# Optimization experiments

Measured on AMD Instinct MI355X. Metric: run time of the kernel, lower is better.

## Reference

```python
import jax, jax.numpy as jnp
import numpy as np

VOCAB_SIZE = 32000


def setup_inputs() -> dict:
    key = jax.random.key(0)
    k1, k2, k3, k4 = jax.random.split(key, 4)
    B, S, T, H = 4, 512, 256, 1024
    return {
        "inputs": jax.random.randint(k1, (B, S), 0, VOCAB_SIZE, dtype=jnp.int32),
        "encoder_outputs": jax.random.normal(k2, (B, S, H), dtype=jnp.float32),
        "decoder_outputs": jax.random.normal(k3, (B, T, H), dtype=jnp.float32),
        "input_bias": jnp.zeros((B, S), dtype=jnp.float32),
        "W_proj": jax.random.normal(k4, (H, H), dtype=jnp.float32) * (1.0 / np.sqrt(H)),
        "b_proj": jnp.zeros((H,), dtype=jnp.float32),
    }


def reference(inputs, encoder_outputs, decoder_outputs, input_bias, W_proj, b_proj):
    # copy_projection: Dense(hidden) with tanh activation on encoder outputs
    enc = jnp.tanh(jnp.einsum("bsh,hk->bsk", encoder_outputs, W_proj) + b_proj)
    # decoder-encoder scores: [B, T, S]
    scores = jnp.einsum("bth,bsh->bts", decoder_outputs, enc)
    scores = scores + input_bias[:, None, :]  # bias broadcast over target dim
    probs = jax.nn.softmax(scores, axis=-1)  # [B, T, S]

    # map_updates_to_vocab: scatter-add probs into vocab slots by token id
    def scatter_one(p, ids):  # p: [T, S], ids: [S]
        return jnp.zeros((p.shape[0], VOCAB_SIZE), p.dtype).at[:, ids].add(p)

    copy_probs = jax.vmap(scatter_one)(probs, inputs)  # [B, T, V]
    return copy_probs
```

## Files before the change

kernel.cpp:

```cpp
#include <hip/hip_runtime.h>
#include <hip/hip_bf16.h>
#include <math.h>

typedef __bf16 bf16x8 __attribute__((ext_vector_type(8)));
typedef float  f32x4  __attribute__((ext_vector_type(4)));

__device__ __forceinline__ unsigned short f2bf(float x) {
    unsigned u = __float_as_uint(x);
    u += 0x7fffu + ((u >> 16) & 1u);
    return (unsigned short)(u >> 16);
}
__device__ __forceinline__ float bf2f(unsigned short h) {
    return __uint_as_float(((unsigned)h) << 16);
}

__device__ __forceinline__ void gl2lds16(const void* g, void* l) {
    __builtin_amdgcn_global_load_lds(
        (const __attribute__((address_space(1))) unsigned int*)(uintptr_t)g,
        (__attribute__((address_space(3))) unsigned int*)(unsigned int)(uintptr_t)l,
        16, 0, 0);
}

__global__ __launch_bounds__(256) void prep(const float* __restrict__ encf,
                                            unsigned short* __restrict__ eh,
                                            unsigned short* __restrict__ el,
                                            const float* __restrict__ decf,
                                            unsigned short* __restrict__ dh,
                                            unsigned short* __restrict__ dl,
                                            const float* __restrict__ W,
                                            unsigned short* __restrict__ Wth,
                                            unsigned short* __restrict__ Wtl) {
    const int bid = blockIdx.x;
    if (bid < 3072) {
        const float* src; unsigned short *ph, *pl; int i;
        if (bid < 2048) { src = encf; ph = eh; pl = el; i = bid * 256 + threadIdx.x; }
        else            { src = decf; ph = dh; pl = dl; i = (bid - 2048) * 256 + threadIdx.x; }
        const float4 v = ((const float4*)src)[i];
        ushort4 h, l;
        h.x = f2bf(v.x); l.x = f2bf(v.x - bf2f(h.x));
        h.y = f2bf(v.y); l.y = f2bf(v.y - bf2f(h.y));
        h.z = f2bf(v.z); l.z = f2bf(v.z - bf2f(h.z));
        h.w = f2bf(v.w); l.w = f2bf(v.w - bf2f(h.w));
        ((ushort4*)ph)[i] = h;
        ((ushort4*)pl)[i] = l;
        return;
    }
    __shared__ float tile[64][65];
    const int tb = bid - 3072;
    const int k0 = (tb >> 4) * 64, n0 = (tb & 15) * 64;
    const int c = threadIdx.x & 63, r0 = threadIdx.x >> 6;
    #pragma unroll
    for (int p = 0; p < 16; ++p) {
        int r = r0 + p * 4;
        tile[r][c] = W[(size_t)(k0 + r) * 1024 + n0 + c];
    }
    __syncthreads();
    #pragma unroll
    for (int p = 0; p < 16; ++p) {
        int rn = r0 + p * 4;
        float v = tile[c][rn];
        unsigned short h = f2bf(v);
        size_t idx = (size_t)(n0 + rn) * 1024 + k0 + c;
        Wth[idx] = h;
        Wtl[idx] = f2bf(v - bf2f(h));
    }
}

template <int EPI>
__global__ __launch_bounds__(256) void gemm128(
    const unsigned short* __restrict__ Ah, const unsigned short* __restrict__ Al,
    const unsigned short* __restrict__ Bh, const unsigned short* __restrict__ Bl,
    const float* __restrict__ bias,
    float* __restrict__ Cf, unsigned short* __restrict__ Ch, unsigned short* __restrict__ Cl,
    int N, int K, int kIter, int ksplit,
    long long aBatch, long long bBatch, long long cBatch, long long cPart) {

    const int z = blockIdx.z;
    const int batch = z / ksplit;
    const int ks = z - batch * ksplit;
    Ah += (size_t)batch * aBatch;  Al += (size_t)batch * aBatch;
    Bh += (size_t)batch * bBatch;  Bl += (size_t)batch * bBatch;
    const int kOff = ks * kIter * 32;

    __shared__ __align__(16) unsigned short sAh[128 * 32];
    __shared__ __align__(16) unsigned short sAl[128 * 32];
    __shared__ __align__(16) unsigned short sBh[128 * 32];
    __shared__ __align__(16) unsigned short sBl[128 * 32];

    const int t = threadIdx.x;
    const int lane = t & 63;
    const int w = t >> 6;
    const int wm = w >> 1, wn = w & 1;
    const int ln15 = lane & 15, q4 = lane >> 4;

    const int row0 = blockIdx.y * 128;
    const int col0 = blockIdx.x * 128;

    const int c0 = t,        r0s = c0 >> 2, g0 = ((c0 & 3) ^ (r0s & 3) ^ ((r0s >> 2) & 3)) * 8;
    const int c1 = t + 256,  r1s = c1 >> 2, g1 = ((c1 & 3) ^ (r1s & 3) ^ ((r1s >> 2) & 3)) * 8;
    const size_t a0 = (size_t)(row0 + r0s) * K + kOff + g0;
    const size_t a1 = (size_t)(row0 + r1s) * K + kOff + g1;
    const size_t b0 = (size_t)(col0 + r0s) * K + kOff + g0;
    const size_t b1 = (size_t)(col0 + r1s) * K + kOff + g1;

    const int pq = (q4 ^ (ln15 & 3) ^ ((ln15 >> 2) & 3)) * 8;

    f32x4 acc[4][4] = {};

    for (int kk = 0; kk < kIter; ++kk) {
        const int k0 = kk * 32;
        gl2lds16(Ah + a0 + k0, &sAh[c0 * 8]);
        gl2lds16(Ah + a1 + k0, &sAh[c1 * 8]);
        gl2lds16(Al + a0 + k0, &sAl[c0 * 8]);
        gl2lds16(Al + a1 + k0, &sAl[c1 * 8]);
        gl2lds16(Bh + b0 + k0, &sBh[c0 * 8]);
        gl2lds16(Bh + b1 + k0, &sBh[c1 * 8]);
        gl2lds16(Bl + b0 + k0, &sBl[c0 * 8]);
        gl2lds16(Bl + b1 + k0, &sBl[c1 * 8]);
        __syncthreads();

        bf16x8 ah[4], al[4], bh[4], bl[4];
        #pragma unroll
        for (int i = 0; i < 4; ++i) {
            int rr = wm * 64 + i * 16 + ln15;
            ah[i] = *(const bf16x8*)&sAh[rr * 32 + pq];
            al[i] = *(const bf16x8*)&sAl[rr * 32 + pq];
        }
        #pragma unroll
        for (int j = 0; j < 4; ++j) {
            int rr = wn * 64 + j * 16 + ln15;
            bh[j] = *(const bf16x8*)&sBh[rr * 32 + pq];
            bl[j] = *(const bf16x8*)&sBl[rr * 32 + pq];
        }
        #pragma unroll
        for (int i = 0; i < 4; ++i)
            #pragma unroll
            for (int j = 0; j < 4; ++j) {
                acc[i][j] = __builtin_amdgcn_mfma_f32_16x16x32_bf16(ah[i], bh[j], acc[i][j], 0, 0, 0);
                acc[i][j] = __builtin_amdgcn_mfma_f32_16x16x32_bf16(ah[i], bl[j], acc[i][j], 0, 0, 0);
                acc[i][j] = __builtin_amdgcn_mfma_f32_16x16x32_bf16(al[i], bh[j], acc[i][j], 0, 0, 0);
            }
        __syncthreads();
    }

    float* outp = (EPI == 0) ? (Cf + (size_t)batch * cBatch + (size_t)ks * cPart) : nullptr;
    #pragma unroll
    for (int i = 0; i < 4; ++i)
        #pragma unroll
        for (int j = 0; j < 4; ++j) {
            int colg = col0 + wn * 64 + j * 16 + ln15;
            float bv = (EPI == 1) ? bias[colg] : 0.0f;
            #pragma unroll
            for (int r = 0; r < 4; ++r) {
                int rowg = row0 + wm * 64 + i * 16 + q4 * 4 + r;
                if (EPI == 0) {
                    outp[(size_t)rowg * N + colg] = acc[i][j][r];
                } else {
                    float tv = tanhf(acc[i][j][r] + bv);
                    unsigned short h = f2bf(tv);
                    size_t idx = (size_t)rowg * N + colg;
                    Ch[idx] = h;
                    Cl[idx] = f2bf(tv - bf2f(h));
                }
            }
        }
}

__inline__ __device__ float waveReduceMax(float v) {
    #pragma unroll
    for (int off = 32; off > 0; off >>= 1) v = fmaxf(v, __shfl_down(v, off));
    return v;
}
__inline__ __device__ float waveReduceSum(float v) {
    #pragma unroll
    for (int off = 32; off > 0; off >>= 1) v += __shfl_down(v, off);
    return v;
}

__global__ __launch_bounds__(256) void softmax_scatter(const float* __restrict__ scores,
                                                       const int* __restrict__ tokens,
                                                       const float* __restrict__ ibias,
                                                       float* __restrict__ out) {
    const int row = blockIdx.x;
    const int b = row >> 8;
    const size_t plane = (size_t)4 * 256 * 512;
    const float* s0 = scores + (size_t)row * 512;
    const float* bi = ibias + (size_t)b * 512;
    const int* tok = tokens + (size_t)b * 512;
    float* o = out + (size_t)row * 32000;

    __shared__ float red[4];
    const int tid = threadIdx.x;
    const int wid = tid >> 6, lane = tid & 63;

    float v0 = bi[tid], v1 = bi[tid + 256];
    #pragma unroll
    for (int p = 0; p < 4; ++p) {
        v0 += s0[p * plane + tid];
        v1 += s0[p * plane + tid + 256];
    }

    float m = fmaxf(v0, v1);
    m = waveReduceMax(m);
    if (lane == 0) red[wid] = m;
    __syncthreads();
    if (tid == 0) red[0] = fmaxf(fmaxf(red[0], red[1]), fmaxf(red[2], red[3]));
    __syncthreads();
    const float rowmax = red[0];
    __syncthreads();

    float e0 = __expf(v0 - rowmax);
    float e1 = __expf(v1 - rowmax);
    float s = e0 + e1;
    s = waveReduceSum(s);
    if (lane == 0) red[wid] = s;
    __syncthreads();
    if (tid == 0) red[0] = red[0] + red[1] + red[2] + red[3];
    __syncthreads();
    const float inv = 1.0f / red[0];

    float4 z = make_float4(0.f, 0.f, 0.f, 0.f);
    float4* o4 = (float4*)o;
    for (int i = tid; i < 8000; i += 256) o4[i] = z;

    __threadfence_block();
    __syncthreads();

    atomicAdd(&o[tok[tid]],       e0 * inv);
    atomicAdd(&o[tok[tid + 256]], e1 * inv);
}

extern "C" void kernel_launch(void* const* d_in, const int* in_sizes, int n_in,
                              void* d_out, int out_size, void* d_ws, size_t ws_size,
                              hipStream_t stream) {
    const int*   inputs  = (const int*)d_in[0];
    const float* enc_in  = (const float*)d_in[1];
    const float* dec_in  = (const float*)d_in[2];
    const float* ibias   = (const float*)d_in[3];
    const float* W       = (const float*)d_in[4];
    const float* bproj   = (const float*)d_in[5];
    float* out = (float*)d_out;

    float* scores = (float*)d_ws;

    size_t outBytes = (size_t)out_size * sizeof(float);
    char* tail = (char*)d_out + outBytes - (size_t)24 * 1024 * 1024;
    unsigned short* Aeh = (unsigned short*)tail;
    unsigned short* Ael = Aeh + (size_t)2048 * 1024;
    unsigned short* Dh  = Ael + (size_t)2048 * 1024;
    unsigned short* Dl  = Dh  + (size_t)1024 * 1024;
    unsigned short* Wth = Dl  + (size_t)1024 * 1024;
    unsigned short* Wtl = Wth + (size_t)1024 * 1024;
    unsigned short* ench = Wtl + (size_t)1024 * 1024;
    unsigned short* encl = ench + (size_t)2048 * 1024;

    prep<<<dim3(3328), 256, 0, stream>>>(enc_in, Aeh, Ael, dec_in, Dh, Dl, W, Wth, Wtl);

    gemm128<1><<<dim3(8, 16, 1), 256, 0, stream>>>(
        Aeh, Ael, Wth, Wtl, bproj, nullptr, ench, encl,
        1024, 1024, 32, 1, 0LL, 0LL, 0LL, 0LL);

    gemm128<0><<<dim3(4, 2, 16), 256, 0, stream>>>(
        Dh, Dl, ench, encl, nullptr, scores, nullptr, nullptr,
        512, 1024, 8, 4,
        (long long)256 * 1024, (long long)512 * 1024,
        (long long)256 * 512, (long long)4 * 256 * 512);

    softmax_scatter<<<dim3(4 * 256), 256, 0, stream>>>(scores, inputs, ibias, out);
}
```

Before: 242.0 us.

## Replace LDS-staged GEMM with direct global-to-register MFMA fragment loads

Both split-bf16 GEMMs now skip shared memory. Each wave loads its MFMA fragments directly from global memory, on a new tiling of 256x32 per block and 64x32 per wave, with two k-steps unrolled and no barriers. This removes the LDS staging and the syncthreads cost and gives more blocks. In exchange, data reuse across waves drops, so global and L2 traffic per FLOP rises, and the 16-byte row-strided loads may coalesce poorly.

```diff
diff --git a/kernel.cpp b/kernel.cpp
--- a/kernel.cpp
+++ b/kernel.cpp
@@ -12,13 +12,6 @@
 }
 __device__ __forceinline__ float bf2f(unsigned short h) {
     return __uint_as_float(((unsigned)h) << 16);
-}
-
-__device__ __forceinline__ void gl2lds16(const void* g, void* l) {
-    __builtin_amdgcn_global_load_lds(
-        (const __attribute__((address_space(1))) unsigned int*)(uintptr_t)g,
-        (__attribute__((address_space(3))) unsigned int*)(unsigned int)(uintptr_t)l,
-        16, 0, 0);
 }
 
 __global__ __launch_bounds__(256) void prep(const float* __restrict__ encf,
@@ -66,8 +59,39 @@
     }
 }
 
+struct Frags {
+    bf16x8 ah[4], al[4], bh[2], bl[2];
+};
+
+__device__ __forceinline__ void loadFrags(Frags& f,
+    const unsigned short* pa, const unsigned short* pal,
+    const unsigned short* pb, const unsigned short* pbl,
+    int K, int off) {
+    #pragma unroll
+    for (int i = 0; i < 4; ++i) {
+        f.ah[i] = *(const bf16x8*)(pa  + (size_t)i * 16 * K + off);
+        f.al[i] = *(const bf16x8*)(pal + (size_t)i * 16 * K + off);
+    }
+    #pragma unroll
+    for (int j = 0; j < 2; ++j) {
+        f.bh[j] = *(const bf16x8*)(pb  + (size_t)j * 16 * K + off);
+        f.bl[j] = *(const bf16x8*)(pbl + (size_t)j * 16 * K + off);
+    }
+}
+
+__device__ __forceinline__ void mfmaFrags(f32x4 acc[4][2], const Frags& f) {
+    #pragma unroll
+    for (int i = 0; i < 4; ++i)
+        #pragma unroll
+        for (int j = 0; j < 2; ++j) {
+            acc[i][j] = __builtin_amdgcn_mfma_f32_16x16x32_bf16(f.ah[i], f.bh[j], acc[i][j], 0, 0, 0);
+            acc[i][j] = __builtin_amdgcn_mfma_f32_16x16x32_bf16(f.ah[i], f.bl[j], acc[i][j], 0, 0, 0);
+            acc[i][j] = __builtin_amdgcn_mfma_f32_16x16x32_bf16(f.al[i], f.bh[j], acc[i][j], 0, 0, 0);
+        }
+}
+
 template <int EPI>
-__global__ __launch_bounds__(256) void gemm128(
+__global__ __launch_bounds__(256) void gemm_direct(
     const unsigned short* __restrict__ Ah, const unsigned short* __restrict__ Al,
     const unsigned short* __restrict__ Bh, const unsigned short* __restrict__ Bl,
     const float* __restrict__ bias,
@@ -82,77 +106,39 @@
     Bh += (size_t)batch * bBatch;  Bl += (size_t)batch * bBatch;
     const int kOff = ks * kIter * 32;
 
-    __shared__ __align__(16) unsigned short sAh[128 * 32];
-    __shared__ __align__(16) unsigned short sAl[128 * 32];
-    __shared__ __align__(16) unsigned short sBh[128 * 32];
-    __shared__ __align__(16) unsigned short sBl[128 * 32];
-
     const int t = threadIdx.x;
     const int lane = t & 63;
     const int w = t >> 6;
-    const int wm = w >> 1, wn = w & 1;
     const int ln15 = lane & 15, q4 = lane >> 4;
 
-    const int row0 = blockIdx.y * 128;
-    const int col0 = blockIdx.x * 128;
-
-    const int c0 = t,        r0s = c0 >> 2, g0 = ((c0 & 3) ^ (r0s & 3) ^ ((r0s >> 2) & 3)) * 8;
-    const int c1 = t + 256,  r1s = c1 >> 2, g1 = ((c1 & 3) ^ (r1s & 3) ^ ((r1s >> 2) & 3)) * 8;
-    const size_t a0 = (size_t)(row0 + r0s) * K + kOff + g0;
-    const size_t a1 = (size_t)(row0 + r1s) * K + kOff + g1;
-    const size_t b0 = (size_t)(col0 + r0s) * K + kOff + g0;
-    const size_t b1 = (size_t)(col0 + r1s) * K + kOff + g1;
-
-    const int pq = (q4 ^ (ln15 & 3) ^ ((ln15 >> 2) & 3)) * 8;
-
-    f32x4 acc[4][4] = {};
-
-    for (int kk = 0; kk < kIter; ++kk) {
-        const int k0 = kk * 32;
-        gl2lds16(Ah + a0 + k0, &sAh[c0 * 8]);
-        gl2lds16(Ah + a1 + k0, &sAh[c1 * 8]);
-        gl2lds16(Al + a0 + k0, &sAl[c0 * 8]);
-        gl2lds16(Al + a1 + k0, &sAl[c1 * 8]);
-        gl2lds16(Bh + b0 + k0, &sBh[c0 * 8]);
-        gl2lds16(Bh + b1 + k0, &sBh[c1 * 8]);
-        gl2lds16(Bl + b0 + k0, &sBl[c0 * 8]);
-        gl2lds16(Bl + b1 + k0, &sBl[c1 * 8]);
-        __syncthreads();
-
-        bf16x8 ah[4], al[4], bh[4], bl[4];
-        #pragma unroll
-        for (int i = 0; i < 4; ++i) {
-            int rr = wm * 64 + i * 16 + ln15;
-            ah[i] = *(const bf16x8*)&sAh[rr * 32 + pq];
-            al[i] = *(const bf16x8*)&sAl[rr * 32 + pq];
-        }
-        #pragma unroll
-        for (int j = 0; j < 4; ++j) {
-            int rr = wn * 64 + j * 16 + ln15;
-            bh[j] = *(const bf16x8*)&sBh[rr * 32 + pq];
-            bl[j] = *(const bf16x8*)&sBl[rr * 32 + pq];
-        }
-        #pragma unroll
-        for (int i = 0; i < 4; ++i)
-            #pragma unroll
-            for (int j = 0; j < 4; ++j) {
-                acc[i][j] = __builtin_amdgcn_mfma_f32_16x16x32_bf16(ah[i], bh[j], acc[i][j], 0, 0, 0);
-                acc[i][j] = __builtin_amdgcn_mfma_f32_16x16x32_bf16(ah[i], bl[j], acc[i][j], 0, 0, 0);
-                acc[i][j] = __builtin_amdgcn_mfma_f32_16x16x32_bf16(al[i], bh[j], acc[i][j], 0, 0, 0);
-            }
-        __syncthreads();
+    const int row0 = blockIdx.y * 256 + w * 64;
+    const int col0 = blockIdx.x * 32;
+
+    const unsigned short* pa  = Ah + (size_t)(row0 + ln15) * K + kOff + q4 * 8;
+    const unsigned short* pal = Al + (size_t)(row0 + ln15) * K + kOff + q4 * 8;
+    const unsigned short* pb  = Bh + (size_t)(col0 + ln15) * K + kOff + q4 * 8;
+    const unsigned short* pbl = Bl + (size_t)(col0 + ln15) * K + kOff + q4 * 8;
+
+    f32x4 acc[4][2] = {};
+
+    for (int kk = 0; kk < kIter; kk += 2) {
+        Frags f0, f1;
+        loadFrags(f0, pa, pal, pb, pbl, K, kk * 32);
+        loadFrags(f1, pa, pal, pb, pbl, K, kk * 32 + 32);
+        mfmaFrags(acc, f0);
+        mfmaFrags(acc, f1);
     }
 
     float* outp = (EPI == 0) ? (Cf + (size_t)batch * cBatch + (size_t)ks * cPart) : nullptr;
     #pragma unroll
     for (int i = 0; i < 4; ++i)
         #pragma unroll
-        for (int j = 0; j < 4; ++j) {
-            int colg = col0 + wn * 64 + j * 16 + ln15;
+        for (int j = 0; j < 2; ++j) {
+            int colg = col0 + j * 16 + ln15;
             float bv = (EPI == 1) ? bias[colg] : 0.0f;
             #pragma unroll
             for (int r = 0; r < 4; ++r) {
-                int rowg = row0 + wm * 64 + i * 16 + q4 * 4 + r;
+                int rowg = row0 + i * 16 + q4 * 4 + r;
                 if (EPI == 0) {
                     outp[(size_t)rowg * N + colg] = acc[i][j][r];
                 } else {
@@ -256,11 +242,11 @@
 
     prep<<<dim3(3328), 256, 0, stream>>>(enc_in, Aeh, Ael, dec_in, Dh, Dl, W, Wth, Wtl);
 
-    gemm128<1><<<dim3(8, 16, 1), 256, 0, stream>>>(
+    gemm_direct<1><<<dim3(32, 8, 1), 256, 0, stream>>>(
         Aeh, Ael, Wth, Wtl, bproj, nullptr, ench, encl,
         1024, 1024, 32, 1, 0LL, 0LL, 0LL, 0LL);
 
-    gemm128<0><<<dim3(4, 2, 16), 256, 0, stream>>>(
+    gemm_direct<0><<<dim3(16, 1, 16), 256, 0, stream>>>(
         Dh, Dl, ench, encl, nullptr, scores, nullptr, nullptr,
         512, 1024, 8, 4,
         (long long)256 * 1024, (long long)512 * 1024,
```

New measurement: 254.9 us. 5.4% more time.
